# Performance work log

Measured on AMD Instinct MI355X. Metric: run time of the kernel, lower is better.

The kernel has to match this reference:

```python
import jax, jax.numpy as jnp
import numpy as np

B, S, D, H, FF = 2, 2048, 1024, 16, 4096
DK = D // H
LOCAL_WINDOW, STRIDE = 128, 128
NEG = -1000000000.0
EPS = 1e-5


def _layernorm(x, g, b):
    mu = jnp.mean(x, axis=-1, keepdims=True)
    var = jnp.mean(jnp.square(x - mu), axis=-1, keepdims=True)
    return (x - mu) * jax.lax.rsqrt(var + EPS) * g + b


def _strided_mask(seq):
    # allowed(i, j): j <= i and (i-j <= local_window or (i-j) % stride == 0)
    i = jnp.arange(seq)[:, None]
    j = jnp.arange(seq)[None, :]
    d = i - j
    return (d >= 0) & ((d <= LOCAL_WINDOW) | (d % STRIDE == 0))  # [S, S] bool


def setup_inputs() -> dict:
    key = jax.random.key(0)
    ks = jax.random.split(key, 18)
    w = lambda k, shape: jax.random.normal(k, shape, jnp.float32) * 0.02
    return {
        "x": jax.random.normal(ks[0], (B, S, D), jnp.float32),
        "mask": jnp.ones((1, 1, S, S), jnp.int32),
        "Wq": w(ks[1], (D, D)), "bq": jnp.zeros((D,), jnp.float32),
        "Wk": w(ks[2], (D, D)), "bk": jnp.zeros((D,), jnp.float32),
        "Wv": w(ks[3], (D, D)), "bv": jnp.zeros((D,), jnp.float32),
        "Wo": w(ks[4], (D, D)), "bo": jnp.zeros((D,), jnp.float32),
        "W1": w(ks[5], (D, FF)), "bf1": jnp.zeros((FF,), jnp.float32),
        "W2": w(ks[6], (FF, D)), "bf2": jnp.zeros((D,), jnp.float32),
        "g1": jnp.ones((D,), jnp.float32), "bl1": jnp.zeros((D,), jnp.float32),
        "g2": jnp.ones((D,), jnp.float32), "bl2": jnp.zeros((D,), jnp.float32),
    }


def reference(x, mask, Wq, bq, Wk, bk, Wv, bv, Wo, bo,
              W1, bf1, W2, bf2, g1, bl1, g2, bl2):
    b, s, d = x.shape
    sm = _strided_mask(s)[None, None]  # [1,1,S,S]

    # pre-LN self-attention
    n = _layernorm(x, g1, bl1)
    split = lambda t: t.reshape(b, s, H, DK).transpose(0, 2, 1, 3)  # [B,H,S,DK]
    q = split(n @ Wq + bq)
    k = split(n @ Wk + bk)
    v = split(n @ Wv + bv)

    scores = jnp.einsum('bhqd,bhkd->bhqk', q, k) / jnp.sqrt(jnp.float32(DK))
    scores = jnp.where(sm, scores, NEG)          # strided/local mask
    scores = jnp.where(mask == 0, NEG, scores)   # user mask
    attn = jax.nn.softmax(scores, axis=-1)
    o = jnp.einsum('bhqk,bhkd->bhqd', attn, v)
    o = o.transpose(0, 2, 1, 3).reshape(b, s, d) @ Wo + bo
    x = x + o

    # pre-LN FFN (GELU exact, matching torch nn.GELU default)
    n2 = _layernorm(x, g2, bl2)
    ff = jax.nn.gelu(n2 @ W1 + bf1, approximate=False) @ W2 + bf2
    return x + ff
```

## Files before the change

### kernel.cpp

```cpp
#include <hip/hip_runtime.h>
#include <math.h>

typedef unsigned int u32;
typedef unsigned short u16;

#define B_  2
#define S_  2048
#define D_  1024
#define H_  16
#define DK_ 64
#define FF_ 4096
#define NEG_ -1000000000.0f

typedef __attribute__((ext_vector_type(8))) short short8;
typedef __attribute__((ext_vector_type(4))) float floatx4;
typedef __attribute__((ext_vector_type(4))) unsigned short ushort4_t;

__device__ inline u16 f2b(float f) {
    union { float f; u32 u; } v; v.f = f;
    u32 r = (v.u + 0x7fffu + ((v.u >> 16) & 1u)) >> 16;
    return (u16)r;
}
__device__ inline float b2f(u16 b) {
    union { u32 u; float f; } v; v.u = ((u32)b) << 16;
    return v.f;
}

__device__ inline void gl_lds16(const u16* g, u16* l) {
    __builtin_amdgcn_global_load_lds((const __attribute__((address_space(1))) u32*)g,
                                     (__attribute__((address_space(3))) u32*)l, 16, 0, 0);
}

__global__ void tconv4(const float* __restrict__ W0, const float* __restrict__ W1_,
                       const float* __restrict__ W2_, const float* __restrict__ W3,
                       u16* __restrict__ dstBase) {
    __shared__ float tile[32][33];
    int z = blockIdx.z;
    const float* Wm = (z == 0) ? W0 : (z == 1) ? W1_ : (z == 2) ? W2_ : W3;
    u16* Wt = dstBase + (size_t)z * 1024 * 1024;
    const int K = 1024, N = 1024;
    int n0 = blockIdx.x * 32, k0 = blockIdx.y * 32;
    int tx = threadIdx.x & 31, ty = threadIdx.x >> 5;
#pragma unroll
    for (int r = 0; r < 32; r += 8)
        tile[ty + r][tx] = Wm[(size_t)(k0 + ty + r) * N + n0 + tx];
    __syncthreads();
#pragma unroll
    for (int r = 0; r < 32; r += 8)
        Wt[(size_t)(n0 + ty + r) * K + k0 + tx] = f2b(tile[tx][ty + r]);
}

__global__ void tconv(const float* __restrict__ Wm, u16* __restrict__ Wt, int K, int N) {
    __shared__ float tile[32][33];
    int n0 = blockIdx.x * 32, k0 = blockIdx.y * 32;
    int tx = threadIdx.x & 31, ty = threadIdx.x >> 5;
#pragma unroll
    for (int r = 0; r < 32; r += 8)
        tile[ty + r][tx] = Wm[(size_t)(k0 + ty + r) * N + n0 + tx];
    __syncthreads();
#pragma unroll
    for (int r = 0; r < 32; r += 8)
        Wt[(size_t)(n0 + ty + r) * K + k0 + tx] = f2b(tile[tx][ty + r]);
}

__global__ void catbias(const float* __restrict__ bq, const float* __restrict__ bk,
                        const float* __restrict__ bv, float* __restrict__ out) {
    int i = blockIdx.x * 256 + threadIdx.x;
    float v = (i < 1024) ? bq[i] : (i < 2048) ? bk[i - 1024] : bv[i - 2048];
    out[i] = v;
}

__global__ __launch_bounds__(256)
void mask_tiles(const int* __restrict__ mask, int* __restrict__ tflag) {
    int jt = blockIdx.x, it = blockIdx.y;
    const int* base = mask + (size_t)it * 128 * S_ + jt * 128;
    int t = threadIdx.x;
    int ok = 1;
    for (int e = t; e < 128 * 32; e += 256) {
        int r = e >> 5, c4 = e & 31;
        int4 vv = *(const int4*)&base[(size_t)r * S_ + c4 * 4];
        ok &= (vv.x != 0) & (vv.y != 0) & (vv.z != 0) & (vv.w != 0);
    }
    ok = (int)__all(ok);
    __shared__ int red[4];
    if ((t & 63) == 0) red[t >> 6] = ok;
    __syncthreads();
    if (t == 0) tflag[it * 16 + jt] = red[0] & red[1] & red[2] & red[3];
}

__global__ __launch_bounds__(256)
void ln_bf16(const float* __restrict__ x, const float* __restrict__ g,
             const float* __restrict__ b, u16* __restrict__ out) {
    int row = blockIdx.x, t = threadIdx.x;
    int lane = t & 63, w = t >> 6;
    const float* xr = x + (size_t)row * D_;
    __shared__ float red[8];
    int col0 = t * 4;
    float4 xv = *(const float4*)&xr[col0];
    float v0 = xv.x, v1 = xv.y, v2 = xv.z, v3 = xv.w;
    float s = v0 + v1 + v2 + v3;
    s += __shfl_xor(s, 1); s += __shfl_xor(s, 2); s += __shfl_xor(s, 4);
    s += __shfl_xor(s, 8); s += __shfl_xor(s, 16); s += __shfl_xor(s, 32);
    if (lane == 0) red[w] = s;
    __syncthreads();
    float mu = (red[0] + red[1] + red[2] + red[3]) * (1.0f / D_);
    float d0 = v0 - mu, d1 = v1 - mu, d2 = v2 - mu, d3 = v3 - mu;
    float vs = d0 * d0 + d1 * d1 + d2 * d2 + d3 * d3;
    vs += __shfl_xor(vs, 1); vs += __shfl_xor(vs, 2); vs += __shfl_xor(vs, 4);
    vs += __shfl_xor(vs, 8); vs += __shfl_xor(vs, 16); vs += __shfl_xor(vs, 32);
    if (lane == 0) red[4 + w] = vs;
    __syncthreads();
    float rstd = rsqrtf((red[4] + red[5] + red[6] + red[7]) * (1.0f / D_) + 1e-5f);
    float4 gv = *(const float4*)&g[col0];
    float4 bv = *(const float4*)&b[col0];
    ushort4_t o;
    o[0] = f2b(d0 * rstd * gv.x + bv.x);
    o[1] = f2b(d1 * rstd * gv.y + bv.y);
    o[2] = f2b(d2 * rstd * gv.z + bv.z);
    o[3] = f2b(d3 * rstd * gv.w + bv.w);
    *(ushort4_t*)&out[(size_t)row * D_ + col0] = o;
}

__global__ __launch_bounds__(256)
void merge_ln(const u16* __restrict__ P, const float* __restrict__ x,
              const float* __restrict__ bo, const float* __restrict__ g,
              const float* __restrict__ bl, float* __restrict__ x1,
              u16* __restrict__ n2) {
    const size_t MN = (size_t)B_ * S_ * D_;
    int row = blockIdx.x, t = threadIdx.x;
    int lane = t & 63, w = t >> 6;
    size_t base = (size_t)row * D_;
    __shared__ float red[8];
    int col0 = t * 4;
    float4 xv = *(const float4*)&x[base + col0];
    float4 bv = *(const float4*)&bo[col0];
    ushort4_t p0 = *(const ushort4_t*)&P[base + col0];
    ushort4_t p1 = *(const ushort4_t*)&P[MN + base + col0];
    float v0 = xv.x + bv.x + b2f(p0[0]) + b2f(p1[0]);
    float v1 = xv.y + bv.y + b2f(p0[1]) + b2f(p1[1]);
    float v2 = xv.z + bv.z + b2f(p0[2]) + b2f(p1[2]);
    float v3 = xv.w + bv.w + b2f(p0[3]) + b2f(p1[3]);
    float s = v0 + v1 + v2 + v3;
    s += __shfl_xor(s, 1); s += __shfl_xor(s, 2); s += __shfl_xor(s, 4);
    s += __shfl_xor(s, 8); s += __shfl_xor(s, 16); s += __shfl_xor(s, 32);
    if (lane == 0) red[w] = s;
    __syncthreads();
    float mu = (red[0] + red[1] + red[2] + red[3]) * (1.0f / D_);
    float d0 = v0 - mu, d1 = v1 - mu, d2 = v2 - mu, d3 = v3 - mu;
    float vs = d0 * d0 + d1 * d1 + d2 * d2 + d3 * d3;
    vs += __shfl_xor(vs, 1); vs += __shfl_xor(vs, 2); vs += __shfl_xor(vs, 4);
    vs += __shfl_xor(vs, 8); vs += __shfl_xor(vs, 16); vs += __shfl_xor(vs, 32);
    if (lane == 0) red[4 + w] = vs;
    __syncthreads();
    float rstd = rsqrtf((red[4] + red[5] + red[6] + red[7]) * (1.0f / D_) + 1e-5f);
    float4 gv = *(const float4*)&g[col0];
    float4 blv = *(const float4*)&bl[col0];
    *(float4*)&x1[base + col0] = (float4){v0, v1, v2, v3};
    ushort4_t o;
    o[0] = f2b(d0 * rstd * gv.x + blv.x);
    o[1] = f2b(d1 * rstd * gv.y + blv.y);
    o[2] = f2b(d2 * rstd * gv.z + blv.z);
    o[3] = f2b(d3 * rstd * gv.w + blv.w);
    *(ushort4_t*)&n2[base + col0] = o;
}

template <int EPI>
__global__ __launch_bounds__(256, 4)
void gemm_bt(const u16* __restrict__ A, const u16* __restrict__ Bt,
             const float* __restrict__ bias, const float* __restrict__ R,
             void* __restrict__ Cv, int M, int N, int K, int ldA, int ldB) {
    __shared__ u16 As[2][128 * 32];
    __shared__ u16 Bs[2][128 * 32];
    int tid = threadIdx.x;
    int lane = tid & 63, w = tid >> 6;
    int wm = w >> 1, wn = w & 1;
    int nMt = gridDim.x, nwg = gridDim.x * gridDim.y;
    int id = blockIdx.x + nMt * blockIdx.y;
    int qq = nwg >> 3;
    int sid = (id & 7) * qq + (id >> 3);
    int m0 = (sid % nMt) * 128, n0 = (sid / nMt) * 128;
    size_t koff = (size_t)blockIdx.z * K;

    floatx4 acc[4][4];
#pragma unroll
    for (int a = 0; a < 4; a++)
#pragma unroll
        for (int b2 = 0; b2 < 4; b2++) acc[a][b2] = (floatx4){0.f, 0.f, 0.f, 0.f};

    int r4 = lane >> 2;
    int qg = ((lane & 3) ^ ((lane >> 3) & 3)) * 8;
    const u16* Ag0 = A + (size_t)(m0 + w * 16 + r4) * ldA + koff + qg;
    const u16* Bg0 = Bt + (size_t)(n0 + w * 16 + r4) * ldB + koff + qg;
    const int ldsOff = (w * 16) * 32;

    int c = lane & 15, g = lane >> 4;
    int sw = (g ^ ((c >> 1) & 3)) * 8;

    const int nIter = K >> 5;

    gl_lds16(Ag0, &As[0][ldsOff]);
    gl_lds16(Ag0 + (size_t)64 * ldA, &As[0][ldsOff + 64 * 32]);
    gl_lds16(Bg0, &Bs[0][ldsOff]);
    gl_lds16(Bg0 + (size_t)64 * ldB, &Bs[0][ldsOff + 64 * 32]);

    for (int it = 0; it < nIter; it++) {
        __syncthreads();
        int cur = it & 1, nxt = cur ^ 1;
        if (it + 1 < nIter) {
            int kk = (it + 1) << 5;
            gl_lds16(Ag0 + kk, &As[nxt][ldsOff]);
            gl_lds16(Ag0 + kk + (size_t)64 * ldA, &As[nxt][ldsOff + 64 * 32]);
            gl_lds16(Bg0 + kk, &Bs[nxt][ldsOff]);
            gl_lds16(Bg0 + kk + (size_t)64 * ldB, &Bs[nxt][ldsOff + 64 * 32]);
        }
        short8 fa[4], fb[4];
#pragma unroll
        for (int a = 0; a < 4; a++)
            fa[a] = *(const short8*)&As[cur][(wm * 64 + a * 16 + c) * 32 + sw];
#pragma unroll
        for (int b2 = 0; b2 < 4; b2++)
            fb[b2] = *(const short8*)&Bs[cur][(wn * 64 + b2 * 16 + c) * 32 + sw];
#pragma unroll
        for (int a = 0; a < 4; a++)
#pragma unroll
            for (int b2 = 0; b2 < 4; b2++)
                acc[a][b2] = __builtin_amdgcn_mfma_f32_16x16x32_bf16(fa[a], fb[b2], acc[a][b2], 0, 0, 0);
    }

    int mb = m0 + wm * 64, nb = n0 + wn * 64;
#pragma unroll
    for (int a = 0; a < 4; a++) {
#pragma unroll
        for (int b2 = 0; b2 < 4; b2++) {
            int mrow = mb + a * 16 + g * 4;
            int ncol = nb + b2 * 16 + c;
            float bv = (EPI == 3) ? 0.f : bias[ncol];
#pragma unroll
            for (int r = 0; r < 4; r++) {
                int m = mrow + r;
                float vvv = acc[a][b2][r] + bv;
                if (EPI == 0) {
                    int which = ncol >> 10, col = ncol & 1023;
                    if (which == 0) vvv *= 0.125f;
                    int bb = m >> 11, ss = m & 2047, hh = col >> 6, dk = col & 63;
                    ((u16*)Cv)[(size_t)which * ((size_t)B_ * S_ * D_) +
                               ((((size_t)bb * H_ + hh) * S_) + ss) * DK_ + dk] = f2b(vvv);
                } else if (EPI == 1) {
                    ((float*)Cv)[(size_t)m * N + ncol] = vvv + R[(size_t)m * N + ncol];
                } else if (EPI == 2) {
                    float u = 0.79788456080286536f * fmaf(0.044715f * vvv, vvv * vvv, vvv);
                    float th = 1.f - 2.f / (1.f + __expf(2.f * u));
                    ((u16*)Cv)[(size_t)m * N + ncol] = f2b(0.5f * vvv * (1.f + th));
                } else {
                    ((u16*)Cv)[(size_t)blockIdx.z * M * N + (size_t)m * N + ncol] = f2b(vvv);
                }
            }
        }
    }
}

#define BARR asm volatile("s_barrier" ::: "memory")

template <int EPI>
__global__ __launch_bounds__(512, 2)
void gemm8(const u16* __restrict__ A, const u16* __restrict__ Bt,
           const float* __restrict__ bias, void* __restrict__ Cv,
           int M, int N, int K, int ldA, int ldB) {
    __shared__ u16 sh2[65536];
    const int tid = threadIdx.x;
    const int lane = tid & 63, w = tid >> 6;
    const int wm = w >> 2, wn = w & 3;
    const int c = lane & 15, g = lane >> 4;
    const int cbase = c * 128 + g * 16;
    const int xo = (c & 7) << 4;

    int nMt = gridDim.x;
    int nwg = gridDim.x * gridDim.y;
    int id = blockIdx.x + nMt * blockIdx.y;
    int qq = nwg >> 3;
    int sid = (id & 7) * qq + (id >> 3);
    int m0 = (sid % nMt) * 256, n0 = (sid / nMt) * 256;
    size_t koff = (size_t)blockIdx.z * K;

    const int nT = K >> 6, nI = nT >> 1;

    const int sr = tid >> 3;
    const int sk = ((tid & 7) * 8) ^ (((tid >> 3) & 7) << 3);
    const u16* gA0 = A + (size_t)(m0 + sr) * ldA + koff + sk;
    const u16* gB0 = Bt + (size_t)(n0 + sr) * ldB + koff + sk;
    const int dst0 = w * 512;

#define STG_A(t_, h_) do { \
    const u16* s_ = gA0 + (size_t)(h_) * 128 * ldA + (t_) * 64; \
    u16* l_ = &sh2[((((t_) & 1) * 2 + (h_)) * 8192) + dst0]; \
    gl_lds16(s_, l_); \
    gl_lds16(s_ + (size_t)64 * ldA, l_ + 4096); \
} while (0)
#define STG_B(t_, h_) do { \
    const u16* s_ = gB0 + (size_t)(h_) * 128 * ldB + (t_) * 64; \
    u16* l_ = &sh2[32768 + ((((t_) & 1) * 2 + (h_)) * 8192) + dst0]; \
    gl_lds16(s_, l_); \
    gl_lds16(s_ + (size_t)64 * ldB, l_ + 4096); \
} while (0)

    short8 fa[8], fb0[4], fb1[4];
    floatx4 acc[2][2][4][2];
#pragma unroll
    for (int i = 0; i < 2; i++)
#pragma unroll
        for (int j = 0; j < 2; j++)
#pragma unroll
            for (int a = 0; a < 4; a++)
#pragma unroll
                for (int b2 = 0; b2 < 2; b2++)
                    acc[i][j][a][b2] = (floatx4){0.f, 0.f, 0.f, 0.f};

#define DS_A(d_, qr_) do { \
    int rb_ = ((d_) * 2 + wm) * 16384; \
    _Pragma("unroll") for (int a_ = 0; a_ < 4; a_++) \
    _Pragma("unroll") for (int k_ = 0; k_ < 2; k_++) { \
        int lin_ = (qr_) * 8192 + a_ * 2048 + cbase + k_ * 64; \
        fa[a_ * 2 + k_] = *(const short8*)((const char*)sh2 + rb_ + (lin_ ^ xo)); } \
} while (0)
#define DS_B(d_, qc_, fb_) do { \
    int rb_ = 65536 + ((d_) * 2 + (wn >> 1)) * 16384; \
    _Pragma("unroll") for (int b_ = 0; b_ < 2; b_++) \
    _Pragma("unroll") for (int k_ = 0; k_ < 2; k_++) { \
        int lin_ = (wn & 1) * 8192 + (qc_) * 4096 + b_ * 2048 + cbase + k_ * 64; \
        fb_[b_ * 2 + k_] = *(const short8*)((const char*)sh2 + rb_ + (lin_ ^ xo)); } \
} while (0)
#define MFMA16(qr_, qc_, fb_) do { \
    __builtin_amdgcn_s_setprio(1); \
    _Pragma("unroll") for (int a_ = 0; a_ < 4; a_++) \
    _Pragma("unroll") for (int b_ = 0; b_ < 2; b_++) \
    _Pragma("unroll") for (int k_ = 0; k_ < 2; k_++) \
        acc[qr_][qc_][a_][b_] = __builtin_amdgcn_mfma_f32_16x16x32_bf16( \
            fa[a_ * 2 + k_], fb_[b_ * 2 + k_], acc[qr_][qc_][a_][b_], 0, 0, 0); \
    __builtin_amdgcn_s_setprio(0); \
} while (0)

    STG_B(0, 0); STG_B(0, 1); STG_A(0, 0); STG_A(0, 1);
    STG_A(1, 0); STG_A(1, 1);
    asm volatile("s_waitcnt vmcnt(4)" ::: "memory");
    BARR;

    for (int it2 = 0; it2 < nI; it2++) {
        const int t1 = 2 * it2 + 1, tn0 = t1 + 1, tn1 = t1 + 2;
        DS_A(0, 0); DS_B(0, 0, fb0);
        STG_B(t1, 0);
        MFMA16(0, 0, fb0); BARR;
        DS_B(0, 1, fb1);
        STG_B(t1, 1);
        MFMA16(0, 1, fb1); BARR;
        DS_A(0, 1);
        if (tn0 < nT) STG_B(tn0, 0);
        MFMA16(1, 1, fb1); BARR;
        if (tn0 < nT) {
            STG_B(tn0, 1);
            asm volatile("s_waitcnt vmcnt(4)" ::: "memory");
        } else {
            asm volatile("s_waitcnt vmcnt(0)" ::: "memory");
        }
        MFMA16(1, 0, fb0); BARR;
        DS_A(1, 0); DS_B(1, 0, fb0);
        if (tn0 < nT) STG_A(tn0, 0);
        MFMA16(0, 0, fb0); BARR;
        DS_B(1, 1, fb1);
        if (tn0 < nT) STG_A(tn0, 1);
        MFMA16(0, 1, fb1); BARR;
        DS_A(1, 1);
        if (tn1 < nT) STG_A(tn1, 0);
        MFMA16(1, 1, fb1); BARR;
        if (tn1 < nT) STG_A(tn1, 1);
        if (it2 + 1 < nI) asm volatile("s_waitcnt vmcnt(4)" ::: "memory");
        MFMA16(1, 0, fb0); BARR;
    }

#pragma unroll
    for (int qr = 0; qr < 2; qr++)
#pragma unroll
        for (int qc = 0; qc < 2; qc++)
#pragma unroll
            for (int a = 0; a < 4; a++)
#pragma unroll
                for (int b2 = 0; b2 < 2; b2++) {
                    int mrow = m0 + wm * 128 + qr * 64 + a * 16 + g * 4;
                    int ncol = n0 + wn * 64 + qc * 32 + b2 * 16 + c;
                    float bv = (EPI == 3) ? 0.f : bias[ncol];
#pragma unroll
                    for (int r = 0; r < 4; r++) {
                        int m = mrow + r;
                        float vvv = acc[qr][qc][a][b2][r] + bv;
                        if (EPI == 0) {
                            int which = ncol >> 10, col = ncol & 1023;
                            if (which == 0) vvv *= 0.125f;
                            int bb = m >> 11, ss = m & 2047, hh = col >> 6, dk = col & 63;
                            ((u16*)Cv)[(size_t)which * ((size_t)B_ * S_ * D_) +
                                       ((((size_t)bb * H_ + hh) * S_) + ss) * DK_ + dk] = f2b(vvv);
                        } else if (EPI == 2) {
                            float u = 0.79788456080286536f * fmaf(0.044715f * vvv, vvv * vvv, vvv);
                            float th = 1.f - 2.f / (1.f + __expf(2.f * u));
                            ((u16*)Cv)[(size_t)m * N + ncol] = f2b(0.5f * vvv * (1.f + th));
                        } else {
                            ((u16*)Cv)[(size_t)blockIdx.z * M * N + (size_t)m * N + ncol] = f2b(vvv);
                        }
                    }
                }
#undef STG_A
#undef STG_B
#undef DS_A
#undef DS_B
#undef MFMA16
}

template <int NP>
__global__ __launch_bounds__(256)
void ffn2_merge(const u16* __restrict__ P, const float* __restrict__ x1,
                const float* __restrict__ bf2, float* __restrict__ out) {
    const size_t MN = (size_t)B_ * S_ * D_;
    int e = (blockIdx.x * 256 + threadIdx.x) * 4;
    float4 xv = *(const float4*)&x1[e];
    float4 bv = *(const float4*)&bf2[e & 1023];
    float o0 = xv.x + bv.x, o1 = xv.y + bv.y, o2 = xv.z + bv.z, o3 = xv.w + bv.w;
#pragma unroll
    for (int z = 0; z < NP; z++) {
        ushort4_t pv = *(const ushort4_t*)&P[z * MN + e];
        o0 += b2f(pv[0]); o1 += b2f(pv[1]); o2 += b2f(pv[2]); o3 += b2f(pv[3]);
    }
    *(float4*)&out[e] = (float4){o0, o1, o2, o3};
}

#define MAXB_ 14
__global__ __launch_bounds__(256)
void attn4(const u16* __restrict__ q, const u16* __restrict__ k,
           const u16* __restrict__ v, const int* __restrict__ mask,
           const int* __restrict__ tileOK, u16* __restrict__ ob) {
    __shared__ u16 sh[19456];
    u16* Kw = sh;
    u16* Qs = sh + 13824;
    u16* Vh = sh + 12800;

    const int bh = blockIdx.x;
    const int i0 = (31 - blockIdx.y) * 64;
    const int b  = bh >> 4, h = bh & 15;
    const int t  = threadIdx.x;
    const int lane = t & 63, w = t >> 6;
    const int c = lane & 15, g = lane >> 4;
    const int g4 = g * 4;
    const int qloc16 = w * 16;

    const u16* qg = q + ((size_t)bh * S_ + i0) * DK_;
    const u16* kg = k + (size_t)bh * S_ * DK_;
    const u16* vg = v + (size_t)bh * S_ * DK_;

    const int wlo = (i0 >= 128) ? i0 - 128 : 0;
    const int wn  = i0 + 64 - wlo;
    const int nb  = (i0 >= 256) ? (i0 >> 7) - 1 : 0;
    const int jb0 = i0 & 127;
    const int dd0 = i0 - wlo;

    bool allOK = true;
    {
        const int* rowf = tileOK + (i0 >> 7) * 16;
        int jt0 = wlo >> 7, jt1 = (i0 + 63) >> 7;
        for (int jt = jt0; jt <= jt1; jt++) allOK &= (rowf[jt] != 0);
        for (int m = 0; m < nb; m++) allOK &= (rowf[m] != 0);
    }

    for (int e = t; e < 64 * 8; e += 256) {
        int row = e >> 3, dc = e & 7;
        *(short8*)&Qs[row * 72 + dc * 8] = *(const short8*)(qg + row * 64 + dc * 8);
    }
    for (int e = t; e < wn * 8; e += 256) {
        int row = e >> 3, dc = e & 7;
        *(short8*)&Kw[row * 72 + dc * 8] = *(const short8*)(kg + (size_t)(wlo + row) * 64 + dc * 8);
    }
    __syncthreads();

    float sbr[MAXB_];
    {
        short8 qv0 = *(const short8*)&Qs[(qloc16 + c) * 72 + g * 8];
        short8 qv1 = *(const short8*)&Qs[(qloc16 + c) * 72 + 32 + g * 8];
#pragma unroll
        for (int m = 0; m < MAXB_; m++) {
            sbr[m] = NEG_;
            if (m < nb) {
                int jrow = jb0 + (m << 7) + qloc16 + c;
                short8 kv0 = *(const short8*)(kg + (size_t)jrow * 64 + g * 8);
                short8 kv1 = *(const short8*)(kg + (size_t)jrow * 64 + 32 + g * 8);
                float p = 0.f;
#pragma unroll
                for (int i = 0; i < 8; i++) {
                    p += b2f((u16)qv0[i]) * b2f((u16)kv0[i]);
                    p += b2f((u16)qv1[i]) * b2f((u16)kv1[i]);
                }
                p += __shfl_xor(p, 16);
                p += __shfl_xor(p, 32);
                if (!allOK && mask[(size_t)(i0 + qloc16 + c) * S_ + jrow] == 0) p = NEG_;
                sbr[m] = p;
            }
        }
    }

    floatx4 sc[12];
#pragma unroll
    for (int ct = 0; ct < 12; ct++) sc[ct] = (floatx4){0.f, 0.f, 0.f, 0.f};
    {
        short8 fa0 = *(const short8*)&Qs[(qloc16 + c) * 72 + g * 8];
        short8 fa1 = *(const short8*)&Qs[(qloc16 + c) * 72 + 32 + g * 8];
#pragma unroll
        for (int ct = 0; ct < 12; ct++) {
            short8 fb0 = *(const short8*)&Kw[(ct * 16 + c) * 72 + g * 8];
            short8 fb1 = *(const short8*)&Kw[(ct * 16 + c) * 72 + 32 + g * 8];
            sc[ct] = __builtin_amdgcn_mfma_f32_16x16x32_bf16(fa0, fb0, sc[ct], 0, 0, 0);
            sc[ct] = __builtin_amdgcn_mfma_f32_16x16x32_bf16(fa1, fb1, sc[ct], 0, 0, 0);
        }
    }

#pragma unroll
    for (int ct = 0; ct < 12; ct++) {
        int cidx = ct * 16 + c;
        int j = wlo + cidx;
#pragma unroll
        for (int r = 0; r < 4; r++) {
            int qloc = qloc16 + g4 + r;
            int d = dd0 + qloc - cidx;
            bool ok = (d >= 0) && (d <= 128);
            if (ok && !allOK) ok = (mask[(size_t)(i0 + qloc) * S_ + j] != 0);
            sc[ct][r] = ok ? sc[ct][r] : NEG_;
        }
    }

    float mv[4], inv[4];
#pragma unroll
    for (int r = 0; r < 4; r++) {
        float bs[MAXB_];
#pragma unroll
        for (int m = 0; m < MAXB_; m++)
            bs[m] = (m < nb) ? __shfl(sbr[m], g4 + r, 64) : NEG_;
        float mm = -1e30f;
#pragma unroll
        for (int ct = 0; ct < 12; ct++) mm = fmaxf(mm, sc[ct][r]);
        mm = fmaxf(mm, __shfl_xor(mm, 1));
        mm = fmaxf(mm, __shfl_xor(mm, 2));
        mm = fmaxf(mm, __shfl_xor(mm, 4));
        mm = fmaxf(mm, __shfl_xor(mm, 8));
#pragma unroll
        for (int m = 0; m < MAXB_; m++)
            if (m < nb) mm = fmaxf(mm, bs[m]);
        float sum = 0.f;
#pragma unroll
        for (int ct = 0; ct < 12; ct++) {
            float e = __expf(sc[ct][r] - mm);
            sc[ct][r] = e;
            sum += e;
        }
        sum += __shfl_xor(sum, 1);
        sum += __shfl_xor(sum, 2);
        sum += __shfl_xor(sum, 4);
        sum += __shfl_xor(sum, 8);
#pragma unroll
        for (int m = 0; m < MAXB_; m++)
            if (m < nb) sum += __expf(bs[m] - mm);
        mv[r] = mm;
        inv[r] = 1.f / sum;
    }

    __syncthreads();
    u16* P = Kw;
#pragma unroll
    for (int ct = 0; ct < 12; ct++)
#pragma unroll
        for (int r = 0; r < 4; r++)
            P[(qloc16 + g4 + r) * 200 + ct * 16 + c] = f2b(sc[ct][r]);

    for (int e = t; e < 768; e += 256) {
        int dc = e / 96, jl = e - dc * 96;
        short8 val = {0, 0, 0, 0, 0, 0, 0, 0};
        if (jl < wn) val = *(const short8*)(vg + (size_t)(wlo + jl) * 64 + dc * 8);
#pragma unroll
        for (int i = 0; i < 8; i++) Vh[(dc * 8 + i) * 104 + jl] = (u16)val[i];
    }
    __syncthreads();

    floatx4 o[4];
#pragma unroll
    for (int nt = 0; nt < 4; nt++) o[nt] = (floatx4){0.f, 0.f, 0.f, 0.f};
#pragma unroll
    for (int ks = 0; ks < 3; ks++) {
        short8 pa = *(const short8*)&P[(qloc16 + c) * 200 + ks * 32 + g * 8];
#pragma unroll
        for (int nt = 0; nt < 4; nt++) {
            short8 vb = *(const short8*)&Vh[(nt * 16 + c) * 104 + ks * 32 + g * 8];
            o[nt] = __builtin_amdgcn_mfma_f32_16x16x32_bf16(pa, vb, o[nt], 0, 0, 0);
        }
    }

    if (wn > 96) {
        __syncthreads();
        for (int e = t; e < 768; e += 256) {
            int dc = e / 96, jl = e - dc * 96;
            int j2 = 96 + jl;
            short8 val = {0, 0, 0, 0, 0, 0, 0, 0};
            if (j2 < wn) val = *(const short8*)(vg + (size_t)(wlo + j2) * 64 + dc * 8);
#pragma unroll
            for (int i = 0; i < 8; i++) Vh[(dc * 8 + i) * 104 + jl] = (u16)val[i];
        }
        __syncthreads();
#pragma unroll
        for (int ks = 0; ks < 3; ks++) {
            short8 pa = *(const short8*)&P[(qloc16 + c) * 200 + 96 + ks * 32 + g * 8];
#pragma unroll
            for (int nt = 0; nt < 4; nt++) {
                short8 vb = *(const short8*)&Vh[(nt * 16 + c) * 104 + ks * 32 + g * 8];
                o[nt] = __builtin_amdgcn_mfma_f32_16x16x32_bf16(pa, vb, o[nt], 0, 0, 0);
            }
        }
    }

#pragma unroll
    for (int m = 0; m < MAXB_; m++) {
        if (m < nb) {
            int vbase = jb0 + (m << 7) + qloc16 + g4;
            u16 vv[4][4];
#pragma unroll
            for (int r = 0; r < 4; r++)
#pragma unroll
                for (int nt = 0; nt < 4; nt++)
                    vv[r][nt] = vg[(size_t)(vbase + r) * 64 + nt * 16 + c];
#pragma unroll
            for (int r = 0; r < 4; r++) {
                float bs = __shfl(sbr[m], g4 + r, 64);
                float pb = __expf(bs - mv[r]);
#pragma unroll
                for (int nt = 0; nt < 4; nt++)
                    o[nt][r] += pb * b2f(vv[r][nt]);
            }
        }
    }

#pragma unroll
    for (int nt = 0; nt < 4; nt++) {
#pragma unroll
        for (int r = 0; r < 4; r++) {
            int qi = i0 + qloc16 + g4 + r;
            ob[((size_t)b * S_ + qi) * D_ + h * 64 + nt * 16 + c] = f2b(o[nt][r] * inv[r]);
        }
    }
}

extern "C" void kernel_launch(void* const* d_in, const int* in_sizes, int n_in,
                              void* d_out, int out_size, void* d_ws, size_t ws_size,
                              hipStream_t stream) {
    const float* x    = (const float*)d_in[0];
    const int*   mask = (const int*)  d_in[1];
    const float* Wq   = (const float*)d_in[2];
    const float* bq   = (const float*)d_in[3];
    const float* Wk   = (const float*)d_in[4];
    const float* bk   = (const float*)d_in[5];
    const float* Wv   = (const float*)d_in[6];
    const float* bv   = (const float*)d_in[7];
    const float* Wo   = (const float*)d_in[8];
    const float* bo   = (const float*)d_in[9];
    const float* W1   = (const float*)d_in[10];
    const float* bf1  = (const float*)d_in[11];
    const float* W2   = (const float*)d_in[12];
    const float* bf2  = (const float*)d_in[13];
    const float* g1   = (const float*)d_in[14];
    const float* bl1  = (const float*)d_in[15];
    const float* g2   = (const float*)d_in[16];
    const float* bl2  = (const float*)d_in[17];

    char* wsb = (char*)d_ws;
    const size_t MB = 1024 * 1024;
    u16*   WtQKV  = (u16*)(wsb + 0);
    u16*   WtO    = (u16*)(wsb + 6 * MB);
    u16*   Wt1    = (u16*)(wsb + 8 * MB);
    u16*   Wt2    = (u16*)(wsb + 16 * MB);
    u16*   n1b    = (u16*)(wsb + 24 * MB);
    u16*   qkv    = (u16*)(wsb + 32 * MB);
    u16*   obb    = (u16*)(wsb + 56 * MB);
    float* x1     = (float*)(wsb + 32 * MB);
    u16*   ff1b   = (u16*)(wsb + 48 * MB);
    u16*   Ppart  = (u16*)(wsb + 82 * MB);
    u16*   PpartO = (u16*)(wsb + 82 * MB);
    float* bcat   = (float*)(wsb + 114 * MB);
    int*   tflag  = (int*)(wsb + 115 * MB);
    u16*   n2b    = n1b;

    const int M = B_ * S_;
    const size_t SZ = (size_t)B_ * S_ * D_;

    mask_tiles<<<dim3(16, 16), 256, 0, stream>>>(mask, tflag);
    tconv4<<<dim3(32, 32, 4), 256, 0, stream>>>(Wq, Wk, Wv, Wo, WtQKV);
    tconv<<<dim3(128, 32), 256, 0, stream>>>(W1, Wt1, 1024, 4096);
    tconv<<<dim3(32, 128), 256, 0, stream>>>(W2, Wt2, 4096, 1024);
    catbias<<<12, 256, 0, stream>>>(bq, bk, bv, bcat);

    ln_bf16<<<M, 256, 0, stream>>>(x, g1, bl1, n1b);

    gemm_bt<0><<<dim3(32, 24), 256, 0, stream>>>(n1b, WtQKV, bcat, nullptr, qkv,
                                                 M, 3072, 1024, 1024, 1024);

    attn4<<<dim3(32, 32), 256, 0, stream>>>(qkv, qkv + SZ, qkv + 2 * SZ, mask, tflag, obb);

    gemm_bt<3><<<dim3(32, 8, 2), 256, 0, stream>>>(obb, WtO, nullptr, nullptr, PpartO,
                                                   M, 1024, 512, 1024, 1024);
    merge_ln<<<M, 256, 0, stream>>>(PpartO, x, bo, g2, bl2, x1, n2b);

    gemm8<2><<<dim3(16, 16, 1), 512, 0, stream>>>(n2b, Wt1, bf1, ff1b,
                                                  M, 4096, 1024, 1024, 1024);

    gemm8<3><<<dim3(16, 4, 4), 512, 0, stream>>>(ff1b, Wt2, nullptr, Ppart,
                                                 M, 1024, 1024, 4096, 4096);
    ffn2_merge<4><<<(int)(SZ / 1024), 256, 0, stream>>>(Ppart, x1, bf2, (float*)d_out);
}
```

Measured before the change: 361.6 us.

## Replace 256x256 gemm8 with 128x128 two-wave double-buffered GEMM for QKV and FFN

Removes the hand-scheduled 512-thread 256x256-tile GEMM and adds a simpler 128-thread kernel with 128x128 tiles, 32-wide K steps and a double-buffered LDS stage. The new kernel now serves the QKV projection and both FFN GEMMs. Smaller tiles give more workgroups and less LDS per block. In exchange, each loaded byte feeds fewer MFMAs, there is a __syncthreads every 32-K step, and the fine-grained interleaving of loads and MFMAs is lost.

```diff
diff --git a/kernel.cpp b/kernel.cpp
--- a/kernel.cpp
+++ b/kernel.cpp
@@ -259,158 +259,94 @@
     }
 }
 
-#define BARR asm volatile("s_barrier" ::: "memory")
-
 template <int EPI>
-__global__ __launch_bounds__(512, 2)
-void gemm8(const u16* __restrict__ A, const u16* __restrict__ Bt,
-           const float* __restrict__ bias, void* __restrict__ Cv,
-           int M, int N, int K, int ldA, int ldB) {
-    __shared__ u16 sh2[65536];
-    const int tid = threadIdx.x;
-    const int lane = tid & 63, w = tid >> 6;
-    const int wm = w >> 2, wn = w & 3;
-    const int c = lane & 15, g = lane >> 4;
-    const int cbase = c * 128 + g * 16;
-    const int xo = (c & 7) << 4;
-
-    int nMt = gridDim.x;
-    int nwg = gridDim.x * gridDim.y;
+__global__ __launch_bounds__(128, 2)
+void gemm_w(const u16* __restrict__ A, const u16* __restrict__ Bt,
+            const float* __restrict__ bias, void* __restrict__ Cv,
+            int M, int N, int K, int ldA, int ldB) {
+    __shared__ u16 As[2][128 * 32];
+    __shared__ u16 Bs[2][128 * 32];
+    int tid = threadIdx.x;
+    int lane = tid & 63, w = tid >> 6;
+    int nMt = gridDim.x, nwg = gridDim.x * gridDim.y;
     int id = blockIdx.x + nMt * blockIdx.y;
     int qq = nwg >> 3;
     int sid = (id & 7) * qq + (id >> 3);
-    int m0 = (sid % nMt) * 256, n0 = (sid / nMt) * 256;
+    int m0 = (sid % nMt) * 128, n0 = (sid / nMt) * 128;
     size_t koff = (size_t)blockIdx.z * K;
 
-    const int nT = K >> 6, nI = nT >> 1;
-
-    const int sr = tid >> 3;
-    const int sk = ((tid & 7) * 8) ^ (((tid >> 3) & 7) << 3);
-    const u16* gA0 = A + (size_t)(m0 + sr) * ldA + koff + sk;
-    const u16* gB0 = Bt + (size_t)(n0 + sr) * ldB + koff + sk;
-    const int dst0 = w * 512;
-
-#define STG_A(t_, h_) do { \
-    const u16* s_ = gA0 + (size_t)(h_) * 128 * ldA + (t_) * 64; \
-    u16* l_ = &sh2[((((t_) & 1) * 2 + (h_)) * 8192) + dst0]; \
-    gl_lds16(s_, l_); \
-    gl_lds16(s_ + (size_t)64 * ldA, l_ + 4096); \
+    floatx4 acc[8][4];
+#pragma unroll
+    for (int a = 0; a < 8; a++)
+#pragma unroll
+        for (int b2 = 0; b2 < 4; b2++) acc[a][b2] = (floatx4){0.f, 0.f, 0.f, 0.f};
+
+    int r4 = lane >> 2;
+    int qg = ((lane & 3) ^ ((lane >> 3) & 3)) * 8;
+    const u16* Ag0 = A + (size_t)(m0 + w * 16 + r4) * ldA + koff + qg;
+    const u16* Bg0 = Bt + (size_t)(n0 + w * 16 + r4) * ldB + koff + qg;
+    const int ldsOff = (w * 16) * 32;
+
+    int c = lane & 15, g = lane >> 4;
+    int sw = (g ^ ((c >> 1) & 3)) * 8;
+
+    const int nIter = K >> 5;
+
+#define STAGE_W(buf_, kk_) do { \
+    _Pragma("unroll") for (int ch = 0; ch < 4; ch++) { \
+        gl_lds16(Ag0 + (kk_) + (size_t)(ch * 32) * ldA, &As[buf_][ldsOff + ch * 32 * 32]); \
+        gl_lds16(Bg0 + (kk_) + (size_t)(ch * 32) * ldB, &Bs[buf_][ldsOff + ch * 32 * 32]); \
+    } \
 } while (0)
-#define STG_B(t_, h_) do { \
-    const u16* s_ = gB0 + (size_t)(h_) * 128 * ldB + (t_) * 64; \
-    u16* l_ = &sh2[32768 + ((((t_) & 1) * 2 + (h_)) * 8192) + dst0]; \
-    gl_lds16(s_, l_); \
-    gl_lds16(s_ + (size_t)64 * ldB, l_ + 4096); \
-} while (0)
-
-    short8 fa[8], fb0[4], fb1[4];
-    floatx4 acc[2][2][4][2];
-#pragma unroll
-    for (int i = 0; i < 2; i++)
-#pragma unroll
-        for (int j = 0; j < 2; j++)
-#pragma unroll
-            for (int a = 0; a < 4; a++)
-#pragma unroll
-                for (int b2 = 0; b2 < 2; b2++)
-                    acc[i][j][a][b2] = (floatx4){0.f, 0.f, 0.f, 0.f};
-
-#define DS_A(d_, qr_) do { \
-    int rb_ = ((d_) * 2 + wm) * 16384; \
-    _Pragma("unroll") for (int a_ = 0; a_ < 4; a_++) \
-    _Pragma("unroll") for (int k_ = 0; k_ < 2; k_++) { \
-        int lin_ = (qr_) * 8192 + a_ * 2048 + cbase + k_ * 64; \
-        fa[a_ * 2 + k_] = *(const short8*)((const char*)sh2 + rb_ + (lin_ ^ xo)); } \
-} while (0)
-#define DS_B(d_, qc_, fb_) do { \
-    int rb_ = 65536 + ((d_) * 2 + (wn >> 1)) * 16384; \
-    _Pragma("unroll") for (int b_ = 0; b_ < 2; b_++) \
-    _Pragma("unroll") for (int k_ = 0; k_ < 2; k_++) { \
-        int lin_ = (wn & 1) * 8192 + (qc_) * 4096 + b_ * 2048 + cbase + k_ * 64; \
-        fb_[b_ * 2 + k_] = *(const short8*)((const char*)sh2 + rb_ + (lin_ ^ xo)); } \
-} while (0)
-#define MFMA16(qr_, qc_, fb_) do { \
-    __builtin_amdgcn_s_setprio(1); \
-    _Pragma("unroll") for (int a_ = 0; a_ < 4; a_++) \
-    _Pragma("unroll") for (int b_ = 0; b_ < 2; b_++) \
-    _Pragma("unroll") for (int k_ = 0; k_ < 2; k_++) \
-        acc[qr_][qc_][a_][b_] = __builtin_amdgcn_mfma_f32_16x16x32_bf16( \
-            fa[a_ * 2 + k_], fb_[b_ * 2 + k_], acc[qr_][qc_][a_][b_], 0, 0, 0); \
-    __builtin_amdgcn_s_setprio(0); \
-} while (0)
-
-    STG_B(0, 0); STG_B(0, 1); STG_A(0, 0); STG_A(0, 1);
-    STG_A(1, 0); STG_A(1, 1);
-    asm volatile("s_waitcnt vmcnt(4)" ::: "memory");
-    BARR;
-
-    for (int it2 = 0; it2 < nI; it2++) {
-        const int t1 = 2 * it2 + 1, tn0 = t1 + 1, tn1 = t1 + 2;
-        DS_A(0, 0); DS_B(0, 0, fb0);
-        STG_B(t1, 0);
-        MFMA16(0, 0, fb0); BARR;
-        DS_B(0, 1, fb1);
-        STG_B(t1, 1);
-        MFMA16(0, 1, fb1); BARR;
-        DS_A(0, 1);
-        if (tn0 < nT) STG_B(tn0, 0);
-        MFMA16(1, 1, fb1); BARR;
-        if (tn0 < nT) {
-            STG_B(tn0, 1);
-            asm volatile("s_waitcnt vmcnt(4)" ::: "memory");
-        } else {
-            asm volatile("s_waitcnt vmcnt(0)" ::: "memory");
-        }
-        MFMA16(1, 0, fb0); BARR;
-        DS_A(1, 0); DS_B(1, 0, fb0);
-        if (tn0 < nT) STG_A(tn0, 0);
-        MFMA16(0, 0, fb0); BARR;
-        DS_B(1, 1, fb1);
-        if (tn0 < nT) STG_A(tn0, 1);
-        MFMA16(0, 1, fb1); BARR;
-        DS_A(1, 1);
-        if (tn1 < nT) STG_A(tn1, 0);
-        MFMA16(1, 1, fb1); BARR;
-        if (tn1 < nT) STG_A(tn1, 1);
-        if (it2 + 1 < nI) asm volatile("s_waitcnt vmcnt(4)" ::: "memory");
-        MFMA16(1, 0, fb0); BARR;
-    }
-
-#pragma unroll
-    for (int qr = 0; qr < 2; qr++)
-#pragma unroll
-        for (int qc = 0; qc < 2; qc++)
-#pragma unroll
-            for (int a = 0; a < 4; a++)
-#pragma unroll
-                for (int b2 = 0; b2 < 2; b2++) {
-                    int mrow = m0 + wm * 128 + qr * 64 + a * 16 + g * 4;
-                    int ncol = n0 + wn * 64 + qc * 32 + b2 * 16 + c;
-                    float bv = (EPI == 3) ? 0.f : bias[ncol];
-#pragma unroll
-                    for (int r = 0; r < 4; r++) {
-                        int m = mrow + r;
-                        float vvv = acc[qr][qc][a][b2][r] + bv;
-                        if (EPI == 0) {
-                            int which = ncol >> 10, col = ncol & 1023;
-                            if (which == 0) vvv *= 0.125f;
-                            int bb = m >> 11, ss = m & 2047, hh = col >> 6, dk = col & 63;
-                            ((u16*)Cv)[(size_t)which * ((size_t)B_ * S_ * D_) +
-                                       ((((size_t)bb * H_ + hh) * S_) + ss) * DK_ + dk] = f2b(vvv);
-                        } else if (EPI == 2) {
-                            float u = 0.79788456080286536f * fmaf(0.044715f * vvv, vvv * vvv, vvv);
-                            float th = 1.f - 2.f / (1.f + __expf(2.f * u));
-                            ((u16*)Cv)[(size_t)m * N + ncol] = f2b(0.5f * vvv * (1.f + th));
-                        } else {
-                            ((u16*)Cv)[(size_t)blockIdx.z * M * N + (size_t)m * N + ncol] = f2b(vvv);
-                        }
-                    }
+
+    STAGE_W(0, 0);
+
+    for (int it = 0; it < nIter; it++) {
+        __syncthreads();
+        int cur = it & 1, nxt = cur ^ 1;
+        if (it + 1 < nIter) STAGE_W(nxt, (it + 1) << 5);
+        short8 fa[8], fb[4];
+#pragma unroll
+        for (int a = 0; a < 8; a++)
+            fa[a] = *(const short8*)&As[cur][(a * 16 + c) * 32 + sw];
+#pragma unroll
+        for (int b2 = 0; b2 < 4; b2++)
+            fb[b2] = *(const short8*)&Bs[cur][(w * 64 + b2 * 16 + c) * 32 + sw];
+#pragma unroll
+        for (int a = 0; a < 8; a++)
+#pragma unroll
+            for (int b2 = 0; b2 < 4; b2++)
+                acc[a][b2] = __builtin_amdgcn_mfma_f32_16x16x32_bf16(fa[a], fb[b2], acc[a][b2], 0, 0, 0);
+    }
+#undef STAGE_W
+
+#pragma unroll
+    for (int a = 0; a < 8; a++) {
+#pragma unroll
+        for (int b2 = 0; b2 < 4; b2++) {
+            int mrow = m0 + a * 16 + g * 4;
+            int ncol = n0 + w * 64 + b2 * 16 + c;
+            float bv = (EPI == 3) ? 0.f : bias[ncol];
+#pragma unroll
+            for (int r = 0; r < 4; r++) {
+                int m = mrow + r;
+                float vvv = acc[a][b2][r] + bv;
+                if (EPI == 0) {
+                    int which = ncol >> 10, col = ncol & 1023;
+                    if (which == 0) vvv *= 0.125f;
+                    int bb = m >> 11, ss = m & 2047, hh = col >> 6, dk = col & 63;
+                    ((u16*)Cv)[(size_t)which * ((size_t)B_ * S_ * D_) +
+                               ((((size_t)bb * H_ + hh) * S_) + ss) * DK_ + dk] = f2b(vvv);
+                } else if (EPI == 2) {
+                    float u = 0.79788456080286536f * fmaf(0.044715f * vvv, vvv * vvv, vvv);
+                    float th = 1.f - 2.f / (1.f + __expf(2.f * u));
+                    ((u16*)Cv)[(size_t)m * N + ncol] = f2b(0.5f * vvv * (1.f + th));
+                } else {
+                    ((u16*)Cv)[(size_t)blockIdx.z * M * N + (size_t)m * N + ncol] = f2b(vvv);
                 }
-#undef STG_A
-#undef STG_B
-#undef DS_A
-#undef DS_B
-#undef MFMA16
+            }
+        }
+    }
 }
 
 template <int NP>
@@ -699,8 +635,8 @@
 
     ln_bf16<<<M, 256, 0, stream>>>(x, g1, bl1, n1b);
 
-    gemm_bt<0><<<dim3(32, 24), 256, 0, stream>>>(n1b, WtQKV, bcat, nullptr, qkv,
-                                                 M, 3072, 1024, 1024, 1024);
+    gemm_w<0><<<dim3(32, 24), 128, 0, stream>>>(n1b, WtQKV, bcat, qkv,
+                                                M, 3072, 1024, 1024, 1024);
 
     attn4<<<dim3(32, 32), 256, 0, stream>>>(qkv, qkv + SZ, qkv + 2 * SZ, mask, tflag, obb);
 
@@ -708,10 +644,10 @@
                                                    M, 1024, 512, 1024, 1024);
     merge_ln<<<M, 256, 0, stream>>>(PpartO, x, bo, g2, bl2, x1, n2b);
 
-    gemm8<2><<<dim3(16, 16, 1), 512, 0, stream>>>(n2b, Wt1, bf1, ff1b,
-                                                  M, 4096, 1024, 1024, 1024);
-
-    gemm8<3><<<dim3(16, 4, 4), 512, 0, stream>>>(ff1b, Wt2, nullptr, Ppart,
-                                                 M, 1024, 1024, 4096, 4096);
+    gemm_w<2><<<dim3(32, 32), 128, 0, stream>>>(n2b, Wt1, bf1, ff1b,
+                                                M, 4096, 1024, 1024, 1024);
+
+    gemm_w<3><<<dim3(32, 8, 4), 128, 0, stream>>>(ff1b, Wt2, nullptr, Ppart,
+                                                  M, 1024, 1024, 4096, 4096);
     ffn2_merge<4><<<(int)(SZ / 1024), 256, 0, stream>>>(Ppart, x1, bf2, (float*)d_out);
 }
```

New measurement: 388.3 us. 7.4% more time.
